# Kernel tuning notes

Hardware: AMD Instinct MI355X
Metric: run time of the kernel (lower is better)

The kernel has to match this reference:

```python
import jax, jax.numpy as jnp
import numpy as np

H, W = 128, 128
K = 16                # num_samples
RADIUS = 2.0
SIGMA = 1.0
EPS = 1e-10
MIN_DEPTH = 1e-6
N = 16384             # number of points
FEAT_DIM = 64
FAR = 1e9             # sentinel pixel coord for invalid (behind-camera) points


def setup_inputs() -> dict:
    key = jax.random.key(0)
    k1, k2, k3, k4, k5 = jax.random.split(key, 5)
    fx = fy = 128.0
    cx = cy = 64.0
    # Back-project uniform pixel locations with z in [1, 5] so points land on the image.
    u = jax.random.uniform(k1, (N,), minval=0.0, maxval=float(W))
    v = jax.random.uniform(k2, (N,), minval=0.0, maxval=float(H))
    z = jax.random.uniform(k3, (N,), minval=1.0, maxval=5.0)
    x = (u - cx) * z / fx
    y = (v - cy) * z / fy
    pcd_points = jnp.stack([x, y, z], axis=-1).astype(jnp.float32)
    pcd_colors = jax.random.uniform(k4, (N, 3), dtype=jnp.float32)
    pcd_feats = jax.random.normal(k5, (N, FEAT_DIM), dtype=jnp.float32)
    intrinsics = jnp.array([[fx, 0.0, cx], [0.0, fy, cy], [0.0, 0.0, 1.0]], dtype=jnp.float32)
    return {"pcd_points": pcd_points, "pcd_colors": pcd_colors,
            "pcd_feats": pcd_feats, "intrinsics": intrinsics}


def _render_pixels(pcd_points, intrinsics):
    # Project to pixel coords (u, v); points behind camera pushed to FAR so kNN never picks them.
    depths = pcd_points[:, 2]
    valid = depths > MIN_DEPTH
    safe_z = jnp.where(valid, depths, 1.0)
    u = pcd_points[:, 0] * intrinsics[0, 0] / safe_z + intrinsics[0, 2]
    v = pcd_points[:, 1] * intrinsics[1, 1] / safe_z + intrinsics[1, 2]
    pix = jnp.stack([u, v], axis=-1)                       # (N, 2)
    pix = jnp.where(valid[:, None], pix, FAR)
    return pix, depths


def _forward(pcd_points, pcd_colors, pcd_feats, intrinsics):
    pix, depths = _render_pixels(pcd_points, intrinsics)
    # Centered pixel grid, row-major flatten: coords are (x+0.5, y+0.5).
    ii, jj = jnp.meshgrid(jnp.arange(H), jnp.arange(W), indexing='ij')
    img_pix = jnp.stack([jj.ravel() + 0.5, ii.ravel() + 0.5], axis=-1).astype(pix.dtype)  # (P, 2)
    # Brute-force 2D kNN: (P, N) squared distances. Indices are non-differentiable.
    d2 = jnp.sum((img_pix[:, None, :] - pix[None, :, :]) ** 2, axis=-1)  # (P, N)
    _, idx = jax.lax.top_k(-jax.lax.stop_gradient(d2), K)                # (P, K)
    # Depth-sort the k neighbors (ascending), as torch.sort on zbuffers.
    zbuf = depths[idx]
    order = jnp.argsort(zbuf, axis=-1)
    idx = jnp.take_along_axis(idx, order, axis=-1)                       # (P, K)
    # Distances of sorted neighbors to the pixel center (differentiable path).
    knn_pix = pix[idx]                                                   # (P, K, 2)
    dist = jnp.linalg.norm(knn_pix - img_pix[:, None, :], axis=-1)       # (P, K)
    masks = dist < RADIUS
    # Exponential weighting + weighted (normalized) compositing.
    w = jnp.exp(-(dist ** 2) / (SIGMA ** 2)) * masks.astype(dist.dtype)
    w = w / (jnp.sum(w, axis=-1, keepdims=True) + EPS)
    sel_depths = depths[idx]                                             # (P, K)
    rendered_depths = jnp.sum(sel_depths * w, axis=-1).reshape(H, W)
    rendered_colors = jnp.sum(pcd_colors[idx] * w[..., None], axis=1).reshape(H, W, 3)
    rendered_feats = jnp.sum(pcd_feats[idx] * w[..., None], axis=1).reshape(H, W, FEAT_DIM)
    rendered_masks = jnp.any(masks, axis=-1).reshape(H, W)
    return rendered_depths, rendered_colors, rendered_feats, rendered_masks


def reference(pcd_points, pcd_colors, pcd_feats, intrinsics):
    return _forward(pcd_points, pcd_colors, pcd_feats, intrinsics)
```

## Files before the change

### kernel.cpp

```cpp
#include <hip/hip_runtime.h>

#define HH 128
#define WW 128
#define HW 16384
#define KK 16
#define NPTS 16384
#define FEAT 64
#define RADIUS2 4.0f
#define EPSV 1e-10f
#define PCAP 48

__global__ void project_expand(const float* __restrict__ pts,
                               const float* __restrict__ intr,
                               int* __restrict__ pix_cnt,
                               float2* __restrict__ pairs) {
    int n = blockIdx.x * blockDim.x + threadIdx.x;
    if (n >= NPTS) return;
    float fx = intr[0], cx = intr[2], fy = intr[4], cy = intr[5];
    float x = pts[3 * n], y = pts[3 * n + 1], z = pts[3 * n + 2];
    if (!(z > 1e-6f)) return;
    float u = x * fx / z + cx;
    float v = y * fy / z + cy;
    int j0 = (int)floorf(u - 2.5f) + 1;
    int i0 = (int)floorf(v - 2.5f) + 1;
    float idf = __int_as_float(n);
#pragma unroll
    for (int di = 0; di < 4; ++di) {
        int i = i0 + di;
        float dv = (float)i + 0.5f - v;
        bool iok = (i >= 0) & (i < HH);
#pragma unroll
        for (int dj = 0; dj < 4; ++dj) {
            int j = j0 + dj;
            float du = (float)j + 0.5f - u;
            float d2 = du * du + dv * dv;
            if (iok && j >= 0 && j < WW && d2 < RADIUS2) {
                int p = i * WW + j;
                int slot = atomicAdd(&pix_cnt[p], 1);
                if (slot < PCAP)
                    pairs[p * PCAP + slot] = make_float2(d2, idf);
            }
        }
    }
}

__global__ __launch_bounds__(64) void render_kernel(
        const float2* __restrict__ pairs,
        const int* __restrict__ pix_cnt,
        const float* __restrict__ pts,
        const float* __restrict__ colors,
        float* __restrict__ out_depth, float* __restrict__ out_colors,
        float* __restrict__ out_mask,
        int* __restrict__ knn_idx, float* __restrict__ knn_w) {
    int tid = threadIdx.x;
    int tile = blockIdx.x;
    int j0 = (tile & 15) * 8;
    int i0 = (tile >> 4) * 4;
    int lp = tid >> 1, lane = tid & 1;
    int li = lp >> 3, lj = lp & 7;
    int p = (i0 + li) * WW + (j0 + lj);

    int cnt = min(pix_cnt[p], PCAP);
    const float2* __restrict__ lst = pairs + p * PCAP;

    float bd[KK];
    int   bt[KK];
#pragma unroll
    for (int k = 0; k < KK; ++k) { bd[k] = 1e30f; bt[k] = -1; }

    for (int base = lane; base < cnt; base += 16) {
        float2 c[8];
        bool   vb[8];
#pragma unroll
        for (int q = 0; q < 8; ++q) {
            int s = base + 2 * q;
            vb[q] = s < cnt;
            c[q] = lst[min(s, cnt - 1)];
        }
#pragma unroll
        for (int q = 0; q < 8; ++q) {
            float dd = vb[q] ? c[q].x : 1e30f;
            int   tt = vb[q] ? __float_as_int(c[q].y) : -1;
#pragma unroll
            for (int k = 0; k < KK; ++k) {
                bool cc = dd < bd[k];
                float nb = cc ? dd : bd[k];
                dd = cc ? bd[k] : dd;
                int nt = cc ? tt : bt[k];
                tt = cc ? bt[k] : tt;
                bd[k] = nb; bt[k] = nt;
            }
        }
    }

    float mb[8]; int mt[8];
#pragma unroll
    for (int k = 0; k < 8; ++k) {
        float obd = __shfl_xor(bd[15 - k], 1);
        int   obt = __shfl_xor(bt[15 - k], 1);
        bool take = obd < bd[k];
        mb[k] = take ? obd : bd[k];
        mt[k] = take ? obt : bt[k];
    }

    float wv[8];
    float wsum_l = 0.f;
#pragma unroll
    for (int k = 0; k < 8; ++k) {
        bool valid = mt[k] >= 0;
        float wk = valid ? __expf(-mb[k]) : 0.f;
        wv[k] = wk; wsum_l += wk;
    }
    float wsum = wsum_l + __shfl_xor(wsum_l, 1);
    float inv = 1.0f / (wsum + EPSV);

    int nn[8];
#pragma unroll
    for (int k = 0; k < 8; ++k) nn[k] = mt[k] >= 0 ? mt[k] : 0;
    float zv[8], cr[8], cg[8], cb[8];
#pragma unroll
    for (int k = 0; k < 8; ++k) {
        zv[k] = pts[3 * nn[k] + 2];
        cr[k] = colors[3 * nn[k]];
        cg[k] = colors[3 * nn[k] + 1];
        cb[k] = colors[3 * nn[k] + 2];
    }

    float dsum = 0.f, c0 = 0.f, c1 = 0.f, c2 = 0.f;
    int   io[8]; float wo[8];
#pragma unroll
    for (int k = 0; k < 8; ++k) {
        float wk = wv[k] * inv;
        io[k] = nn[k];
        wo[k] = wk;
        dsum += zv[k] * wk;
        c0 += cr[k] * wk;
        c1 += cg[k] * wk;
        c2 += cb[k] * wk;
    }

    int4*   ki4 = (int4*)(knn_idx + p * KK + lane * 8);
    float4* kw4 = (float4*)(knn_w + p * KK + lane * 8);
    ki4[0] = make_int4(io[0], io[1], io[2], io[3]);
    ki4[1] = make_int4(io[4], io[5], io[6], io[7]);
    kw4[0] = make_float4(wo[0], wo[1], wo[2], wo[3]);
    kw4[1] = make_float4(wo[4], wo[5], wo[6], wo[7]);

    dsum += __shfl_xor(dsum, 1);
    c0 += __shfl_xor(c0, 1);
    c1 += __shfl_xor(c1, 1);
    c2 += __shfl_xor(c2, 1);

    if (lane == 0) {
        out_depth[p] = dsum;
        out_colors[3 * p]     = c0;
        out_colors[3 * p + 1] = c1;
        out_colors[3 * p + 2] = c2;
        out_mask[p] = (wsum > 0.f) ? 1.0f : 0.0f;
    }
}

__global__ void feats_kernel(const float* __restrict__ feats,
                             const int* __restrict__ knn_idx,
                             const float* __restrict__ knn_w,
                             float* __restrict__ out_feats) {
    int p = blockIdx.x * blockDim.y + threadIdx.y;
    int f = threadIdx.x;
    int nn[KK]; float wk[KK];
#pragma unroll
    for (int k = 0; k < KK; ++k) {
        nn[k] = knn_idx[p * KK + k];
        wk[k] = knn_w[p * KK + k];
    }
    float fv[KK];
#pragma unroll
    for (int k = 0; k < KK; ++k) fv[k] = feats[nn[k] * FEAT + f];
    float acc = 0.f;
#pragma unroll
    for (int k = 0; k < KK; ++k) acc = fmaf(wk[k], fv[k], acc);
    out_feats[p * FEAT + f] = acc;
}

extern "C" void kernel_launch(void* const* d_in, const int* in_sizes, int n_in,
                              void* d_out, int out_size, void* d_ws, size_t ws_size,
                              hipStream_t stream) {
    const float* pts    = (const float*)d_in[0];
    const float* colors = (const float*)d_in[1];
    const float* feats  = (const float*)d_in[2];
    const float* intr   = (const float*)d_in[3];

    float* out = (float*)d_out;
    float* out_depth  = out;
    float* out_colors = out + HW;
    float* out_feats  = out + HW * 4;
    float* out_mask   = out + HW * 68;

    char* ws = (char*)d_ws;
    int* pix_cnt   = (int*)ws;
    float2* pairs  = (float2*)(ws + HW * sizeof(int));
    int* knn_idx   = (int*)(ws + HW * sizeof(int) + (size_t)HW * PCAP * 8);
    float* knn_w   = (float*)((char*)knn_idx + (size_t)HW * KK * 4);

    hipMemsetAsync(pix_cnt, 0, HW * sizeof(int), stream);
    project_expand<<<NPTS / 256, 256, 0, stream>>>(pts, intr, pix_cnt, pairs);
    render_kernel<<<512, 64, 0, stream>>>(pairs, pix_cnt, pts, colors,
                                          out_depth, out_colors, out_mask, knn_idx, knn_w);
    dim3 fb(FEAT, 4);
    feats_kernel<<<HW / 4, fb, 0, stream>>>(feats, knn_idx, knn_w, out_feats);
}
```

Baseline: 93.23 us.

## Fuse kNN render and feature gather into one kernel via shared memory

Merges the render kernel and the feature-compositing kernel into one launch. Each 256-thread block handles an 8x8 pixel tile: 128 threads run the kNN selection and store indices and weights in shared memory, then all 256 threads gather and blend the 64-dim features. This removes one kernel launch and the global round trip for the kNN index and weight buffers. In exchange, half the threads sit idle during selection, and with 256 blocks the GPU may be underfilled, so the gather phase has less parallelism.

```diff
diff --git a/kernel.cpp b/kernel.cpp
--- a/kernel.cpp
+++ b/kernel.cpp
@@ -44,141 +44,133 @@
     }
 }
 
-__global__ __launch_bounds__(64) void render_kernel(
+__global__ __launch_bounds__(256) void render_feats_kernel(
         const float2* __restrict__ pairs,
         const int* __restrict__ pix_cnt,
         const float* __restrict__ pts,
         const float* __restrict__ colors,
+        const float* __restrict__ feats,
         float* __restrict__ out_depth, float* __restrict__ out_colors,
-        float* __restrict__ out_mask,
-        int* __restrict__ knn_idx, float* __restrict__ knn_w) {
+        float* __restrict__ out_feats, float* __restrict__ out_mask) {
+    __shared__ int   kni_s[64][KK];
+    __shared__ float knw_s[64][KK];
+
     int tid = threadIdx.x;
     int tile = blockIdx.x;
     int j0 = (tile & 15) * 8;
-    int i0 = (tile >> 4) * 4;
-    int lp = tid >> 1, lane = tid & 1;
-    int li = lp >> 3, lj = lp & 7;
-    int p = (i0 + li) * WW + (j0 + lj);
+    int i0 = (tile >> 4) * 8;
 
-    int cnt = min(pix_cnt[p], PCAP);
-    const float2* __restrict__ lst = pairs + p * PCAP;
+    if (tid < 128) {
+        int lp = tid >> 1, lane = tid & 1;
+        int li = lp >> 3, lj = lp & 7;
+        int p = (i0 + li) * WW + (j0 + lj);
 
-    float bd[KK];
-    int   bt[KK];
+        int cnt = min(pix_cnt[p], PCAP);
+        const float2* __restrict__ lst = pairs + p * PCAP;
+
+        float bd[KK];
+        int   bt[KK];
 #pragma unroll
-    for (int k = 0; k < KK; ++k) { bd[k] = 1e30f; bt[k] = -1; }
+        for (int k = 0; k < KK; ++k) { bd[k] = 1e30f; bt[k] = -1; }
 
-    for (int base = lane; base < cnt; base += 16) {
-        float2 c[8];
-        bool   vb[8];
+        for (int base = lane; base < cnt; base += 16) {
+            float2 c[8];
+            bool   vb[8];
 #pragma unroll
-        for (int q = 0; q < 8; ++q) {
-            int s = base + 2 * q;
-            vb[q] = s < cnt;
-            c[q] = lst[min(s, cnt - 1)];
-        }
+            for (int q = 0; q < 8; ++q) {
+                int s = base + 2 * q;
+                vb[q] = s < cnt;
+                c[q] = lst[min(s, cnt - 1)];
+            }
 #pragma unroll
-        for (int q = 0; q < 8; ++q) {
-            float dd = vb[q] ? c[q].x : 1e30f;
-            int   tt = vb[q] ? __float_as_int(c[q].y) : -1;
+            for (int q = 0; q < 8; ++q) {
+                float dd = vb[q] ? c[q].x : 1e30f;
+                int   tt = vb[q] ? __float_as_int(c[q].y) : -1;
 #pragma unroll
-            for (int k = 0; k < KK; ++k) {
-                bool cc = dd < bd[k];
-                float nb = cc ? dd : bd[k];
-                dd = cc ? bd[k] : dd;
-                int nt = cc ? tt : bt[k];
-                tt = cc ? bt[k] : tt;
-                bd[k] = nb; bt[k] = nt;
+                for (int k = 0; k < KK; ++k) {
+                    bool cc = dd < bd[k];
+                    float nb = cc ? dd : bd[k];
+                    dd = cc ? bd[k] : dd;
+                    int nt = cc ? tt : bt[k];
+                    tt = cc ? bt[k] : tt;
+                    bd[k] = nb; bt[k] = nt;
+                }
             }
         }
+
+        float mb[8]; int mt[8];
+#pragma unroll
+        for (int k = 0; k < 8; ++k) {
+            float obd = __shfl_xor(bd[15 - k], 1);
+            int   obt = __shfl_xor(bt[15 - k], 1);
+            bool take = obd < bd[k];
+            mb[k] = take ? obd : bd[k];
+            mt[k] = take ? obt : bt[k];
+        }
+
+        float wv[8];
+        float wsum_l = 0.f;
+#pragma unroll
+        for (int k = 0; k < 8; ++k) {
+            bool valid = mt[k] >= 0;
+            float wk = valid ? __expf(-mb[k]) : 0.f;
+            wv[k] = wk; wsum_l += wk;
+        }
+        float wsum = wsum_l + __shfl_xor(wsum_l, 1);
+        float inv = 1.0f / (wsum + EPSV);
+
+        int nn[8];
+#pragma unroll
+        for (int k = 0; k < 8; ++k) nn[k] = mt[k] >= 0 ? mt[k] : 0;
+        float zv[8], cr[8], cg[8], cb[8];
+#pragma unroll
+        for (int k = 0; k < 8; ++k) {
+            zv[k] = pts[3 * nn[k] + 2];
+            cr[k] = colors[3 * nn[k]];
+            cg[k] = colors[3 * nn[k] + 1];
+            cb[k] = colors[3 * nn[k] + 2];
+        }
+
+        float dsum = 0.f, c0 = 0.f, c1 = 0.f, c2 = 0.f;
+#pragma unroll
+        for (int k = 0; k < 8; ++k) {
+            float wk = wv[k] * inv;
+            kni_s[lp][lane * 8 + k] = nn[k];
+            knw_s[lp][lane * 8 + k] = wk;
+            dsum += zv[k] * wk;
+            c0 += cr[k] * wk;
+            c1 += cg[k] * wk;
+            c2 += cb[k] * wk;
+        }
+
+        dsum += __shfl_xor(dsum, 1);
+        c0 += __shfl_xor(c0, 1);
+        c1 += __shfl_xor(c1, 1);
+        c2 += __shfl_xor(c2, 1);
+
+        if (lane == 0) {
+            out_depth[p] = dsum;
+            out_colors[3 * p]     = c0;
+            out_colors[3 * p + 1] = c1;
+            out_colors[3 * p + 2] = c2;
+            out_mask[p] = (wsum > 0.f) ? 1.0f : 0.0f;
+        }
     }
+    __syncthreads();
 
-    float mb[8]; int mt[8];
+    int f = tid & 63;
+    int sl = tid >> 6;
+    for (int q = sl; q < 64; q += 4) {
+        float acc = 0.f;
 #pragma unroll
-    for (int k = 0; k < 8; ++k) {
-        float obd = __shfl_xor(bd[15 - k], 1);
-        int   obt = __shfl_xor(bt[15 - k], 1);
-        bool take = obd < bd[k];
-        mb[k] = take ? obd : bd[k];
-        mt[k] = take ? obt : bt[k];
+        for (int k = 0; k < KK; ++k) {
+            int n = kni_s[q][k];
+            float wk = knw_s[q][k];
+            acc = fmaf(wk, feats[n * FEAT + f], acc);
+        }
+        int p = (i0 + (q >> 3)) * WW + j0 + (q & 7);
+        out_feats[p * FEAT + f] = acc;
     }
-
-    float wv[8];
-    float wsum_l = 0.f;
-#pragma unroll
-    for (int k = 0; k < 8; ++k) {
-        bool valid = mt[k] >= 0;
-        float wk = valid ? __expf(-mb[k]) : 0.f;
-        wv[k] = wk; wsum_l += wk;
-    }
-    float wsum = wsum_l + __shfl_xor(wsum_l, 1);
-    float inv = 1.0f / (wsum + EPSV);
-
-    int nn[8];
-#pragma unroll
-    for (int k = 0; k < 8; ++k) nn[k] = mt[k] >= 0 ? mt[k] : 0;
-    float zv[8], cr[8], cg[8], cb[8];
-#pragma unroll
-    for (int k = 0; k < 8; ++k) {
-        zv[k] = pts[3 * nn[k] + 2];
-        cr[k] = colors[3 * nn[k]];
-        cg[k] = colors[3 * nn[k] + 1];
-        cb[k] = colors[3 * nn[k] + 2];
-    }
-
-    float dsum = 0.f, c0 = 0.f, c1 = 0.f, c2 = 0.f;
-    int   io[8]; float wo[8];
-#pragma unroll
-    for (int k = 0; k < 8; ++k) {
-        float wk = wv[k] * inv;
-        io[k] = nn[k];
-        wo[k] = wk;
-        dsum += zv[k] * wk;
-        c0 += cr[k] * wk;
-        c1 += cg[k] * wk;
-        c2 += cb[k] * wk;
-    }
-
-    int4*   ki4 = (int4*)(knn_idx + p * KK + lane * 8);
-    float4* kw4 = (float4*)(knn_w + p * KK + lane * 8);
-    ki4[0] = make_int4(io[0], io[1], io[2], io[3]);
-    ki4[1] = make_int4(io[4], io[5], io[6], io[7]);
-    kw4[0] = make_float4(wo[0], wo[1], wo[2], wo[3]);
-    kw4[1] = make_float4(wo[4], wo[5], wo[6], wo[7]);
-
-    dsum += __shfl_xor(dsum, 1);
-    c0 += __shfl_xor(c0, 1);
-    c1 += __shfl_xor(c1, 1);
-    c2 += __shfl_xor(c2, 1);
-
-    if (lane == 0) {
-        out_depth[p] = dsum;
-        out_colors[3 * p]     = c0;
-        out_colors[3 * p + 1] = c1;
-        out_colors[3 * p + 2] = c2;
-        out_mask[p] = (wsum > 0.f) ? 1.0f : 0.0f;
-    }
-}
-
-__global__ void feats_kernel(const float* __restrict__ feats,
-                             const int* __restrict__ knn_idx,
-                             const float* __restrict__ knn_w,
-                             float* __restrict__ out_feats) {
-    int p = blockIdx.x * blockDim.y + threadIdx.y;
-    int f = threadIdx.x;
-    int nn[KK]; float wk[KK];
-#pragma unroll
-    for (int k = 0; k < KK; ++k) {
-        nn[k] = knn_idx[p * KK + k];
-        wk[k] = knn_w[p * KK + k];
-    }
-    float fv[KK];
-#pragma unroll
-    for (int k = 0; k < KK; ++k) fv[k] = feats[nn[k] * FEAT + f];
-    float acc = 0.f;
-#pragma unroll
-    for (int k = 0; k < KK; ++k) acc = fmaf(wk[k], fv[k], acc);
-    out_feats[p * FEAT + f] = acc;
 }
 
 extern "C" void kernel_launch(void* const* d_in, const int* in_sizes, int n_in,
@@ -198,13 +190,9 @@
     char* ws = (char*)d_ws;
     int* pix_cnt   = (int*)ws;
     float2* pairs  = (float2*)(ws + HW * sizeof(int));
-    int* knn_idx   = (int*)(ws + HW * sizeof(int) + (size_t)HW * PCAP * 8);
-    float* knn_w   = (float*)((char*)knn_idx + (size_t)HW * KK * 4);
 
     hipMemsetAsync(pix_cnt, 0, HW * sizeof(int), stream);
     project_expand<<<NPTS / 256, 256, 0, stream>>>(pts, intr, pix_cnt, pairs);
-    render_kernel<<<512, 64, 0, stream>>>(pairs, pix_cnt, pts, colors,
-                                          out_depth, out_colors, out_mask, knn_idx, knn_w);
-    dim3 fb(FEAT, 4);
-    feats_kernel<<<HW / 4, fb, 0, stream>>>(feats, knn_idx, knn_w, out_feats);
+    render_feats_kernel<<<256, 256, 0, stream>>>(pairs, pix_cnt, pts, colors, feats,
+                                                 out_depth, out_colors, out_feats, out_mask);
 }
```

Measured after the change: 103.1 us. 10.6% more time.
